# Optimization experiments

Hardware: AMD Instinct MI355X
Metric: run time of the kernel (lower is better)

## Reference

```python
import jax, jax.numpy as jnp
import numpy as np

CONTEXT_LENGTHS = [1, 3, 5, 7]
PADS = [(f - 1) // 2 for f in CONTEXT_LENGTHS]  # p(f) for odd f
B, H, L, DK = 2, 8, 1024, 64
C = H * DK  # conv channels = d_k * n_heads


def _conv1d(x, w, b, pad):
    # x: (b, C, L), w: (C, C, f), b: (C,) -- torch Conv1d semantics
    y = jax.lax.conv_general_dilated(
        x, w, window_strides=(1,), padding=[(pad, pad)],
        dimension_numbers=("NCH", "OIH", "NCH"))
    return y + b[None, :, None]


def _plane(a, w, b, pad, out_len):
    # Faithful to: conv(a.reshape(b, h*d_k, -1)).reshape(b, h, -1, d_k)[:, :, :out_len, :]
    bsz, h, l, d = a.shape
    y = _conv1d(a.reshape(bsz, h * d, l), w, b, pad)
    return y.reshape(bsz, h, -1, d)[:, :, :out_len, :]


def setup_inputs() -> dict:
    key = jax.random.key(0)
    ks = jax.random.split(key, 12)
    inp = {
        "Q": jax.random.normal(ks[0], (B, H, L, DK), jnp.float32),
        "K": jax.random.normal(ks[1], (B, H, L, DK), jnp.float32),
        "V": jax.random.normal(ks[2], (B, H, L, DK), jnp.float32),
        # causal mask: True = masked
        "attn_mask": jnp.broadcast_to(
            jnp.triu(jnp.ones((L, L), jnp.bool_), k=1), (B, H, L, L)),
    }
    for i, f in enumerate(CONTEXT_LENGTHS):
        scale = 1.0 / np.sqrt(C * f)
        inp[f"conv_w{i}"] = jax.random.normal(ks[3 + i], (C, C, f), jnp.float32) * scale
        inp[f"conv_b{i}"] = jax.random.normal(ks[7 + i], (C,), jnp.float32) * scale
    return inp


def reference(Q, K, V, attn_mask,
              conv_w0, conv_b0, conv_w1, conv_b1,
              conv_w2, conv_b2, conv_w3, conv_b3):
    ws = [conv_w0, conv_w1, conv_w2, conv_w3]
    bs = [conv_b0, conv_b1, conv_b2, conv_b3]
    b, h, l, d_k = Q.shape
    l_k = K.shape[2]
    p = len(CONTEXT_LENGTHS)
    Q_l = [_plane(Q, ws[i], bs[i], PADS[i], l) for i in range(p)]
    K_l = [_plane(K, ws[i], bs[i], PADS[i], l_k) for i in range(p)]
    # replicate torch.cat(dim=0).reshape(b, h, p, l, d) exactly (row-major)
    Q_p = jnp.concatenate(Q_l, axis=0).reshape(b, h, p, l, d_k)
    K_p = jnp.concatenate(K_l, axis=0).reshape(b, h, p, l_k, d_k)
    scores = jnp.einsum("bhpqd,bhpkd->bhpqk", Q_p, K_p) / np.sqrt(d_k).astype(np.float32)
    scores = jnp.where(attn_mask[:, :, None, :, :], jnp.float32(-1e9), scores)
    attn = jax.nn.softmax(scores, axis=-1)
    attn = jnp.max(attn, axis=2)  # max over planes -> (b,h,q,k)
    context = jnp.einsum("bhqk,bhkd->bhqd", attn, V)
    return (context, attn)
```

## Files before the change

kernel.cpp:

```cpp
#include <hip/hip_runtime.h>
#include <math.h>

#define C_CH 512
#define L_SEQ 1024
#define DK 64
#define NP 4
#define SC2 0.1803368801111f

typedef __attribute__((ext_vector_type(8))) short short8;
typedef __attribute__((ext_vector_type(4))) float f32x4;

__device__ __forceinline__ unsigned short f2bf(float f) {
    union { float f; unsigned u; } v; v.f = f;
    unsigned u = v.u;
    u += 0x7FFFu + ((u >> 16) & 1u);
    return (unsigned short)(u >> 16);
}

__global__ __launch_bounds__(256)
void prep_w_kernel(const float* __restrict__ w0, const float* __restrict__ w1,
                   const float* __restrict__ w2, const float* __restrict__ w3,
                   unsigned short* __restrict__ Wb) {
    int tg = blockIdx.y;
    int plane, t;
    if (tg < 1)      { plane = 0; t = tg; }
    else if (tg < 4) { plane = 1; t = tg - 1; }
    else if (tg < 9) { plane = 2; t = tg - 4; }
    else             { plane = 3; t = tg - 9; }
    const float* W = (plane == 0) ? w0 : (plane == 1) ? w1 : (plane == 2) ? w2 : w3;
    const int f = (plane == 0) ? 1 : (plane == 1) ? 3 : (plane == 2) ? 5 : 7;

    int co = blockIdx.x * 32 + (threadIdx.x >> 3);
    int c8 = threadIdx.x & 7;
    for (int it = 0; it < 8; it++) {
        int ci = c8 * 8 + it * 64;
        unsigned short o[8];
#pragma unroll
        for (int j = 0; j < 8; j++)
            o[j] = f2bf(W[(size_t)(co * C_CH + ci + j) * f + t]);
        *(short8*)&Wb[((size_t)tg * C_CH + co) * C_CH + ci] = *(short8*)o;
    }
}

__global__ __launch_bounds__(256)
void prep_x_kernel(const float* __restrict__ Qin, const float* __restrict__ Kin,
                   unsigned short* __restrict__ Xt) {
    int tb = blockIdx.z;
    int tensor = tb >> 1, b = tb & 1;
    const float* X = (tensor ? Kin : Qin) + (size_t)b * C_CH * L_SEQ;
    unsigned short* O = Xt + (size_t)tb * 1032 * C_CH;

    int pos0 = blockIdx.x * 64;
    int ci0  = blockIdx.y * 64;
    int tid = threadIdx.x;

    __shared__ float tile[64][65];
    int tx = tid & 15, ty = tid >> 4;
#pragma unroll
    for (int rr = 0; rr < 4; rr++) {
        int ci_l = ty + rr * 16;
        float4 v = *(const float4*)&X[(size_t)(ci0 + ci_l) * L_SEQ + pos0 + tx * 4];
        tile[tx * 4 + 0][ci_l] = v.x;
        tile[tx * 4 + 1][ci_l] = v.y;
        tile[tx * 4 + 2][ci_l] = v.z;
        tile[tx * 4 + 3][ci_l] = v.w;
    }
    __syncthreads();
#pragma unroll
    for (int pp = 0; pp < 2; pp++) {
        int pos_l = (tid >> 3) + pp * 32;
        int cg = (tid & 7) * 8;
        unsigned short o[8];
#pragma unroll
        for (int j = 0; j < 8; j++) o[j] = f2bf(tile[pos_l][cg + j]);
        *(short8*)&O[(size_t)(pos0 + pos_l + 4) * C_CH + ci0 + cg] = *(short8*)o;
    }
    if (blockIdx.x == 0) {
        int r = tid >> 6, cc = tid & 63;
        O[(size_t)r * C_CH + ci0 + cc] = 0;
    }
    if (blockIdx.x == 15) {
        int r = tid >> 6, cc = tid & 63;
        O[(size_t)(1028 + r) * C_CH + ci0 + cc] = 0;
    }
}

__global__ __launch_bounds__(256)
void conv_pair_kernel(const unsigned short* __restrict__ Xt,
                      const unsigned short* __restrict__ Wb,
                      const float* __restrict__ b0, const float* __restrict__ b1,
                      const float* __restrict__ b2, const float* __restrict__ b3,
                      unsigned short* __restrict__ Qp, unsigned short* __restrict__ Kp) {
    const int fs[4]   = {1, 3, 5, 7};
    const int toff[4] = {0, 1, 4, 9};
    int blk = blockIdx.x;
    int cls = blk >> 7;
    int idx = blk & 127;
    int co0  = (idx & 3) * 128;
    int pos0 = ((idx >> 2) & 7) * 128;
    int tb   = idx >> 5;
    int tensor = tb >> 1, b = tb & 1;
    unsigned short* Out = tensor ? Kp : Qp;
    const unsigned short* Xbase = Xt + (size_t)tb * 1032 * C_CH;

    __shared__ __align__(16) unsigned short As[4096];
    __shared__ __align__(16) unsigned short Bs[4096];

    int tid  = threadIdx.x;
    int w    = tid >> 6;
    int lane = tid & 63;
    int l15  = lane & 15;
    int quad = lane >> 4;
    int wm = (w & 1) * 64;
    int wn = (w >> 1) * 64;
    int rowL = tid >> 2;
    int cS   = tid & 3;

    int woff[2];
#pragma unroll
    for (int rep = 0; rep < 2; rep++) {
        int r = rowL + rep * 64;
        int line = r >> 1;
        int sl = (((r & 1) << 2) | cS) ^ (line & 7);
        woff[rep] = line * 64 + sl * 8;
    }
    int aoff[4], boff[4];
#pragma unroll
    for (int mi = 0; mi < 4; mi++) {
        int r = wm + mi * 16 + l15;
        int line = r >> 1;
        aoff[mi] = line * 64 + ((((r & 1) << 2) | quad) ^ (line & 7)) * 8;
        int r2 = wn + mi * 16 + l15;
        int line2 = r2 >> 1;
        boff[mi] = line2 * 64 + ((((r2 & 1) << 2) | quad) ^ (line2 & 7)) * 8;
    }

    for (int ti = 0; ti < 2; ti++) {
        int plane = (cls == 0) ? (ti == 0 ? 0 : 3) : (ti == 0 ? 1 : 2);
        const int f   = fs[plane];
        const int pad = (f - 1) >> 1;
        const float* bias = (plane == 0) ? b0 : (plane == 1) ? b1 : (plane == 2) ? b2 : b3;
        const int n = f * 16;

        f32x4 acc[4][4];
#pragma unroll
        for (int mi = 0; mi < 4; mi++)
#pragma unroll
            for (int ni = 0; ni < 4; ni++) acc[mi][ni] = (f32x4){0.f, 0.f, 0.f, 0.f};

        short8 pA[2], pB[2];
        {
            const unsigned short* Wsl = Wb + ((size_t)toff[plane] * C_CH + co0) * C_CH;
            const unsigned short* Xsl = Xbase + (size_t)(pos0 - pad + 4) * C_CH;
#pragma unroll
            for (int rep = 0; rep < 2; rep++) {
                int r = rowL + rep * 64;
                pA[rep] = *(const short8*)&Wsl[(size_t)r * C_CH + cS * 8];
                pB[rep] = *(const short8*)&Xsl[(size_t)r * C_CH + cS * 8];
            }
        }

        for (int it = 0; it < n; it++) {
            __syncthreads();
            *(short8*)&As[woff[0]] = pA[0];
            *(short8*)&As[woff[1]] = pA[1];
            *(short8*)&Bs[woff[0]] = pB[0];
            *(short8*)&Bs[woff[1]] = pB[1];
            __syncthreads();

            if (it + 1 < n) {
                int t = (it + 1) >> 4, cc = (it + 1) & 15;
                const unsigned short* Wsl =
                    Wb + ((size_t)(toff[plane] + t) * C_CH + co0) * C_CH + cc * 32;
                const unsigned short* Xsl =
                    Xbase + (size_t)(pos0 + t - pad + 4) * C_CH + cc * 32;
#pragma unroll
                for (int rep = 0; rep < 2; rep++) {
                    int r = rowL + rep * 64;
                    pA[rep] = *(const short8*)&Wsl[(size_t)r * C_CH + cS * 8];
                    pB[rep] = *(const short8*)&Xsl[(size_t)r * C_CH + cS * 8];
                }
            }

            short8 af[4], bf[4];
#pragma unroll
            for (int mi = 0; mi < 4; mi++) af[mi] = *(const short8*)&As[aoff[mi]];
#pragma unroll
            for (int ni = 0; ni < 4; ni++) bf[ni] = *(const short8*)&Bs[boff[ni]];
#pragma unroll
            for (int mi = 0; mi < 4; mi++)
#pragma unroll
                for (int ni = 0; ni < 4; ni++)
                    acc[mi][ni] = __builtin_amdgcn_mfma_f32_16x16x32_bf16(
                        af[mi], bf[ni], acc[mi][ni], 0, 0, 0);
        }

#pragma unroll
        for (int mi = 0; mi < 4; mi++)
#pragma unroll
            for (int r = 0; r < 4; r++) {
                int co = co0 + wm + mi * 16 + quad * 4 + r;
                int h = co >> 6, cl = co & 63;
                float bv = bias[co];
                size_t sbase = (size_t)((b * 8 + h) * NP + plane) * L_SEQ * DK;
#pragma unroll
                for (int ni = 0; ni < 4; ni++) {
                    int pos = pos0 + wn + ni * 16 + l15;
                    int l = cl * 16 + (pos >> 6);
                    int d = pos & 63;
                    Out[sbase + (size_t)l * DK + d] = f2bf(acc[mi][ni][r] + bv);
                }
            }
    }
}

__global__ __launch_bounds__(256)
void attn_stats_kernel(const unsigned short* __restrict__ Qb,
                       const unsigned short* __restrict__ Kb,
                       float* __restrict__ pstats) {
    int kc = blockIdx.x, qt = blockIdx.y, bh = blockIdx.z;
    int tid = threadIdx.x;
    size_t pbase = ((size_t)(bh * 16 + qt) * 4 + kc) * (NP * 64);

    if (kc * 4 > qt) { pstats[pbase + tid] = 0.f; return; }

    int q0 = qt * 64;
    int b2 = bh >> 3, h2 = bh & 7;
    int plane  = b2 * 2 + (h2 >> 2);
    int b_orig = (h2 >> 1) & 1;
    int h_base = (h2 & 1) * 4;
    int w = tid >> 6, lane = tid & 63, l15 = lane & 15, quad = lane >> 4;

    const unsigned short* kbase[NP];
    short8 qa[NP][2];
#pragma unroll
    for (int p = 0; p < NP; p++) {
        size_t slice = (size_t)((b_orig * 8 + h_base + p) * NP + plane);
        kbase[p] = Kb + slice * L_SEQ * DK;
        const unsigned short* qrow =
            Qb + (slice * L_SEQ + (size_t)(q0 + w * 16 + l15)) * DK + quad * 8;
        qa[p][0] = *(const short8*)(qrow);
        qa[p][1] = *(const short8*)(qrow + 32);
    }

    float l[NP][4];
#pragma unroll
    for (int p = 0; p < NP; p++)
        for (int r = 0; r < 4; r++) l[p][r] = 0.f;

    int kt1 = min(kc * 4 + 3, qt);
    for (int kt = kc * 4; kt <= kt1; kt++) {
        int k0 = kt * 64;
        bool diag = (kt == qt);
#pragma unroll
        for (int p = 0; p < NP; p++) {
            f32x4 c[4];
#pragma unroll
            for (int s = 0; s < 4; s++) {
                const unsigned short* kr =
                    kbase[p] + (size_t)(k0 + s * 16 + l15) * DK + quad * 8;
                short8 kb0 = *(const short8*)(kr);
                short8 kb1 = *(const short8*)(kr + 32);
                f32x4 acc = {0.f, 0.f, 0.f, 0.f};
                acc = __builtin_amdgcn_mfma_f32_16x16x32_bf16(qa[p][0], kb0, acc, 0, 0, 0);
                acc = __builtin_amdgcn_mfma_f32_16x16x32_bf16(qa[p][1], kb1, acc, 0, 0, 0);
                c[s] = acc;
            }
#pragma unroll
            for (int r = 0; r < 4; r++) {
                int row_local = quad * 4 + r + w * 16;
#pragma unroll
                for (int s = 0; s < 4; s++) {
                    float x = c[s][r] * SC2;
                    if (diag && (s * 16 + l15 > row_local)) x = -1e30f;
                    l[p][r] += exp2f(x);
                }
            }
        }
    }

#pragma unroll
    for (int p = 0; p < NP; p++)
#pragma unroll
        for (int r = 0; r < 4; r++) {
            float ll = l[p][r];
            ll += __shfl_xor(ll, 1);
            ll += __shfl_xor(ll, 2);
            ll += __shfl_xor(ll, 4);
            ll += __shfl_xor(ll, 8);
            if (l15 == 0)
                pstats[pbase + p * 64 + (w * 16 + quad * 4 + r)] = ll;
        }
}

__global__ __launch_bounds__(256)
void attn_combine_kernel(const float* __restrict__ pstats,
                         float* __restrict__ fstats,
                         float* __restrict__ out_ctx) {
    int qt = blockIdx.x, bh = blockIdx.y;
    int tid = threadIdx.x;
    size_t base = ((size_t)(bh * 16 + qt) * 4) * (NP * 64);

    float l = 0.f;
#pragma unroll
    for (int kc = 0; kc < 4; kc++)
        l += pstats[base + (size_t)kc * (NP * 64) + tid];
    fstats[(size_t)(bh * 16 + qt) * (NP * 64) + tid] = __log2f(l);

    int r = tid >> 2, c = (tid & 3) * 16;
    float4 z = make_float4(0.f, 0.f, 0.f, 0.f);
    size_t cbase = ((size_t)bh * L_SEQ + qt * 64 + r) * DK + c;
#pragma unroll
    for (int j = 0; j < 4; j++)
        *(float4*)&out_ctx[cbase + j * 4] = z;
}

__global__ __launch_bounds__(256)
void attn_apply_kernel(const unsigned short* __restrict__ Qb,
                       const unsigned short* __restrict__ Kb,
                       const float* __restrict__ V,
                       const float* __restrict__ fstats,
                       float* __restrict__ out_ctx, float* __restrict__ out_attn) {
    int kc = blockIdx.x, qt = blockIdx.y, bh = blockIdx.z;
    int tid = threadIdx.x;
    int q0 = qt * 64;
    bool any = (kc * 4 <= qt);

    int b2 = bh >> 3, h2 = bh & 7;
    int plane  = b2 * 2 + (h2 >> 2);
    int b_orig = (h2 >> 1) & 1;
    int h_base = (h2 & 1) * 4;
    int w = tid >> 6, lane = tid & 63, l15 = lane & 15, quad = lane >> 4;

    __shared__ float zsm[NP * 64];
    __shared__ __align__(16) unsigned short ast[64 * 80];
    __shared__ __align__(16) unsigned short vts[64 * 80];

    const unsigned short* kbase[NP];
    short8 qa[NP][2];
    if (any) {
        zsm[tid] = fstats[(size_t)(bh * 16 + qt) * (NP * 64) + tid];
#pragma unroll
        for (int p = 0; p < NP; p++) {
            size_t slice = (size_t)((b_orig * 8 + h_base + p) * NP + plane);
            kbase[p] = Kb + slice * L_SEQ * DK;
            const unsigned short* qrow =
                Qb + (slice * L_SEQ + (size_t)(q0 + w * 16 + l15)) * DK + quad * 8;
            qa[p][0] = *(const short8*)(qrow);
            qa[p][1] = *(const short8*)(qrow + 32);
        }
    }

    f32x4 ctxc[4];
#pragma unroll
    for (int ds = 0; ds < 4; ds++) ctxc[ds] = (f32x4){0.f, 0.f, 0.f, 0.f};

    for (int k4 = 0; k4 < 4; k4++) {
        int kt = kc * 4 + k4;
        int k0 = kt * 64;

        if (kt > qt) {
            float4 z = make_float4(0.f, 0.f, 0.f, 0.f);
            size_t abase = ((size_t)bh * L_SEQ + q0) * L_SEQ + k0;
#pragma unroll
            for (int j = 0; j < 4; j++) {
                int flat = tid + j * 256;
                *(float4*)&out_attn[abase + (size_t)(flat >> 4) * L_SEQ + (flat & 15) * 4] = z;
            }
            continue;
        }
        bool diag = (kt == qt);

        __syncthreads();

        {
            int kl = tid >> 2, db = (tid & 3) * 16;
            const float* vr = V + ((size_t)bh * L_SEQ + k0 + kl) * DK + db;
            float vv[16];
            *(float4*)&vv[0]  = *(const float4*)(vr);
            *(float4*)&vv[4]  = *(const float4*)(vr + 4);
            *(float4*)&vv[8]  = *(const float4*)(vr + 8);
            *(float4*)&vv[12] = *(const float4*)(vr + 12);
#pragma unroll
            for (int j = 0; j < 16; j++)
                vts[(db + j) * 80 + kl] = f2bf(vv[j]);
        }

        float run[4][4];
#pragma unroll
        for (int s = 0; s < 4; s++)
            for (int r = 0; r < 4; r++) run[s][r] = -1e30f;

#pragma unroll
        for (int p = 0; p < NP; p++) {
            f32x4 c[4];
#pragma unroll
            for (int s = 0; s < 4; s++) {
                const unsigned short* kr =
                    kbase[p] + (size_t)(k0 + s * 16 + l15) * DK + quad * 8;
                short8 kb0 = *(const short8*)(kr);
                short8 kb1 = *(const short8*)(kr + 32);
                f32x4 acc = {0.f, 0.f, 0.f, 0.f};
                acc = __builtin_amdgcn_mfma_f32_16x16x32_bf16(qa[p][0], kb0, acc, 0, 0, 0);
                acc = __builtin_amdgcn_mfma_f32_16x16x32_bf16(qa[p][1], kb1, acc, 0, 0, 0);
                c[s] = acc;
            }
#pragma unroll
            for (int r = 0; r < 4; r++) {
                float zp = zsm[p * 64 + (quad * 4 + r + w * 16)];
#pragma unroll
                for (int s = 0; s < 4; s++)
                    run[s][r] = fmaxf(run[s][r], c[s][r] * SC2 - zp);
            }
        }

#pragma unroll
        for (int s = 0; s < 4; s++)
#pragma unroll
            for (int r = 0; r < 4; r++) {
                int qloc = w * 16 + quad * 4 + r;
                bool masked = diag && (s * 16 + l15 > qloc);
                float a = masked ? 0.f : exp2f(run[s][r]);
                out_attn[((size_t)bh * L_SEQ + q0 + qloc) * L_SEQ + k0 + s * 16 + l15] = a;
                ast[qloc * 80 + s * 16 + l15] = f2bf(a);
            }
        __syncthreads();

        short8 af0 = *(const short8*)&ast[(w * 16 + l15) * 80 + quad * 8];
        short8 af1 = *(const short8*)&ast[(w * 16 + l15) * 80 + 32 + quad * 8];
#pragma unroll
        for (int ds = 0; ds < 4; ds++) {
            short8 bf0 = *(const short8*)&vts[(ds * 16 + l15) * 80 + quad * 8];
            short8 bf1 = *(const short8*)&vts[(ds * 16 + l15) * 80 + 32 + quad * 8];
            ctxc[ds] = __builtin_amdgcn_mfma_f32_16x16x32_bf16(af0, bf0, ctxc[ds], 0, 0, 0);
            ctxc[ds] = __builtin_amdgcn_mfma_f32_16x16x32_bf16(af1, bf1, ctxc[ds], 0, 0, 0);
        }
    }

    if (any) {
#pragma unroll
        for (int ds = 0; ds < 4; ds++)
#pragma unroll
            for (int r = 0; r < 4; r++) {
                int qg = q0 + w * 16 + quad * 4 + r;
                unsafeAtomicAdd(&out_ctx[((size_t)bh * L_SEQ + qg) * DK + ds * 16 + l15],
                                ctxc[ds][r]);
            }
    }
}

extern "C" void kernel_launch(void* const* d_in, const int* in_sizes, int n_in,
                              void* d_out, int out_size, void* d_ws, size_t ws_size,
                              hipStream_t stream) {
    const float* Q  = (const float*)d_in[0];
    const float* K  = (const float*)d_in[1];
    const float* V  = (const float*)d_in[2];
    const float* w0 = (const float*)d_in[4];
    const float* b0 = (const float*)d_in[5];
    const float* w1 = (const float*)d_in[6];
    const float* b1 = (const float*)d_in[7];
    const float* w2 = (const float*)d_in[8];
    const float* b2 = (const float*)d_in[9];
    const float* w3 = (const float*)d_in[10];
    const float* b3 = (const float*)d_in[11];

    char* ws = (char*)d_ws;
    unsigned short* Wb = (unsigned short*)(ws);
    unsigned short* Xt = (unsigned short*)(ws + 8388608);
    unsigned short* Qp = (unsigned short*)(ws + 12615680);
    unsigned short* Kp = (unsigned short*)(ws + 21004288);
    float* pstats = (float*)(ws + 8388608);
    float* fstats = (float*)(ws + 8388608 + 1048576);

    float* out_ctx  = (float*)d_out;
    float* out_attn = out_ctx + 1048576;

    prep_w_kernel<<<dim3(16, 16), 256, 0, stream>>>(w0, w1, w2, w3, Wb);
    prep_x_kernel<<<dim3(16, 8, 4), 256, 0, stream>>>(Q, K, Xt);
    conv_pair_kernel<<<dim3(256), 256, 0, stream>>>(Xt, Wb, b0, b1, b2, b3, Qp, Kp);
    attn_stats_kernel<<<dim3(4, 16, 16), 256, 0, stream>>>(Qp, Kp, pstats);
    attn_combine_kernel<<<dim3(16, 16), 256, 0, stream>>>(pstats, fstats, out_ctx);
    attn_apply_kernel<<<dim3(4, 16, 16), 256, 0, stream>>>(Qp, Kp, V, fstats,
                                                           out_ctx, out_attn);
}
```

Before: 365.6 us.

## Split conv per plane with double-buffered LDS, triangular tile grids for attention

The conv kernel now launches one block per plane tile (512 blocks) instead of pairing planes per block, and double-buffers the LDS A/B tiles so only one barrier per K-step is needed. Both attention kernels switch to a triangular grid over (q-tile, k-tile) pairs, which skips fully masked tiles instead of launching and early-exiting them. Row sums are now accumulated with atomics into a memset buffer, and the upper-triangle zeroing of the attention output moves into the combine kernel. This adds more atomics and an extra memset in exchange for better load balance and more parallelism.

```diff
diff --git a/kernel.cpp b/kernel.cpp
--- a/kernel.cpp
+++ b/kernel.cpp
@@ -15,6 +15,14 @@
     unsigned u = v.u;
     u += 0x7FFFu + ((u >> 16) & 1u);
     return (unsigned short)(u >> 16);
+}
+
+__device__ __forceinline__ void unpack_tri(int t, int& qt, int& kt) {
+    int q = (int)((sqrtf(8.f * t + 1.f) - 1.f) * 0.5f);
+    while ((q + 1) * (q + 2) / 2 <= t) q++;
+    while (q * (q + 1) / 2 > t) q--;
+    qt = q;
+    kt = t - q * (q + 1) / 2;
 }
 
 __global__ __launch_bounds__(256)
@@ -86,25 +94,32 @@
 }
 
 __global__ __launch_bounds__(256)
-void conv_pair_kernel(const unsigned short* __restrict__ Xt,
+void conv_mfma_kernel(const unsigned short* __restrict__ Xt,
                       const unsigned short* __restrict__ Wb,
                       const float* __restrict__ b0, const float* __restrict__ b1,
                       const float* __restrict__ b2, const float* __restrict__ b3,
                       unsigned short* __restrict__ Qp, unsigned short* __restrict__ Kp) {
     const int fs[4]   = {1, 3, 5, 7};
     const int toff[4] = {0, 1, 4, 9};
-    int blk = blockIdx.x;
-    int cls = blk >> 7;
-    int idx = blk & 127;
-    int co0  = (idx & 3) * 128;
-    int pos0 = ((idx >> 2) & 7) * 128;
-    int tb   = idx >> 5;
+    int id = blockIdx.x;
+    int plane, rel;
+    if (id < 128)      { plane = 0; rel = id; }
+    else if (id < 256) { plane = 1; rel = id - 128; }
+    else if (id < 384) { plane = 3; rel = id - 256; }
+    else               { plane = 2; rel = id - 384; }
+    int co0  = (rel & 3) * 128;
+    int pos0 = ((rel >> 2) & 7) * 128;
+    int tb   = rel >> 5;
     int tensor = tb >> 1, b = tb & 1;
+    const int f   = fs[plane];
+    const int pad = (f - 1) >> 1;
+    const int n   = f * 16;
+    const float* bias = (plane == 0) ? b0 : (plane == 1) ? b1 : (plane == 2) ? b2 : b3;
     unsigned short* Out = tensor ? Kp : Qp;
     const unsigned short* Xbase = Xt + (size_t)tb * 1032 * C_CH;
 
-    __shared__ __align__(16) unsigned short As[4096];
-    __shared__ __align__(16) unsigned short Bs[4096];
+    __shared__ __align__(16) unsigned short As[2][4096];
+    __shared__ __align__(16) unsigned short Bs[2][4096];
 
     int tid  = threadIdx.x;
     int w    = tid >> 6;
@@ -135,23 +150,38 @@
         boff[mi] = line2 * 64 + ((((r2 & 1) << 2) | quad) ^ (line2 & 7)) * 8;
     }
 
-    for (int ti = 0; ti < 2; ti++) {
-        int plane = (cls == 0) ? (ti == 0 ? 0 : 3) : (ti == 0 ? 1 : 2);
-        const int f   = fs[plane];
-        const int pad = (f - 1) >> 1;
-        const float* bias = (plane == 0) ? b0 : (plane == 1) ? b1 : (plane == 2) ? b2 : b3;
-        const int n = f * 16;
-
-        f32x4 acc[4][4];
-#pragma unroll
-        for (int mi = 0; mi < 4; mi++)
-#pragma unroll
-            for (int ni = 0; ni < 4; ni++) acc[mi][ni] = (f32x4){0.f, 0.f, 0.f, 0.f};
-
-        short8 pA[2], pB[2];
-        {
-            const unsigned short* Wsl = Wb + ((size_t)toff[plane] * C_CH + co0) * C_CH;
-            const unsigned short* Xsl = Xbase + (size_t)(pos0 - pad + 4) * C_CH;
+    f32x4 acc[4][4];
+#pragma unroll
+    for (int mi = 0; mi < 4; mi++)
+#pragma unroll
+        for (int ni = 0; ni < 4; ni++) acc[mi][ni] = (f32x4){0.f, 0.f, 0.f, 0.f};
+
+    short8 pA[2], pB[2];
+    {
+        const unsigned short* Wsl = Wb + ((size_t)toff[plane] * C_CH + co0) * C_CH;
+        const unsigned short* Xsl = Xbase + (size_t)(pos0 - pad + 4) * C_CH;
+#pragma unroll
+        for (int rep = 0; rep < 2; rep++) {
+            int r = rowL + rep * 64;
+            pA[rep] = *(const short8*)&Wsl[(size_t)r * C_CH + cS * 8];
+            pB[rep] = *(const short8*)&Xsl[(size_t)r * C_CH + cS * 8];
+        }
+    }
+
+    for (int it = 0; it < n; it++) {
+        int cur = it & 1;
+        *(short8*)&As[cur][woff[0]] = pA[0];
+        *(short8*)&As[cur][woff[1]] = pA[1];
+        *(short8*)&Bs[cur][woff[0]] = pB[0];
+        *(short8*)&Bs[cur][woff[1]] = pB[1];
+        __syncthreads();
+
+        if (it + 1 < n) {
+            int t = (it + 1) >> 4, cc = (it + 1) & 15;
+            const unsigned short* Wsl =
+                Wb + ((size_t)(toff[plane] + t) * C_CH + co0) * C_CH + cc * 32;
+            const unsigned short* Xsl =
+                Xbase + (size_t)(pos0 + t - pad + 4) * C_CH + cc * 32;
 #pragma unroll
             for (int rep = 0; rep < 2; rep++) {
                 int r = rowL + rep * 64;
@@ -160,76 +190,152 @@
             }
         }
 
-        for (int it = 0; it < n; it++) {
-            __syncthreads();
-            *(short8*)&As[woff[0]] = pA[0];
-            *(short8*)&As[woff[1]] = pA[1];
-            *(short8*)&Bs[woff[0]] = pB[0];
-            *(short8*)&Bs[woff[1]] = pB[1];
-            __syncthreads();
-
-            if (it + 1 < n) {
-                int t = (it + 1) >> 4, cc = (it + 1) & 15;
-                const unsigned short* Wsl =
-                    Wb + ((size_t)(toff[plane] + t) * C_CH + co0) * C_CH + cc * 32;
-                const unsigned short* Xsl =
-                    Xbase + (size_t)(pos0 + t - pad + 4) * C_CH + cc * 32;
-#pragma unroll
-                for (int rep = 0; rep < 2; rep++) {
-                    int r = rowL + rep * 64;
-                    pA[rep] = *(const short8*)&Wsl[(size_t)r * C_CH + cS * 8];
-                    pB[rep] = *(const short8*)&Xsl[(size_t)r * C_CH + cS * 8];
-                }
+        short8 af[4], bf[4];
+#pragma unroll
+        for (int mi = 0; mi < 4; mi++) af[mi] = *(const short8*)&As[cur][aoff[mi]];
+#pragma unroll
+        for (int ni = 0; ni < 4; ni++) bf[ni] = *(const short8*)&Bs[cur][boff[ni]];
+#pragma unroll
+        for (int mi = 0; mi < 4; mi++)
+#pragma unroll
+            for (int ni = 0; ni < 4; ni++)
+                acc[mi][ni] = __builtin_amdgcn_mfma_f32_16x16x32_bf16(
+                    af[mi], bf[ni], acc[mi][ni], 0, 0, 0);
+    }
+
+#pragma unroll
+    for (int mi = 0; mi < 4; mi++)
+#pragma unroll
+        for (int r = 0; r < 4; r++) {
+            int co = co0 + wm + mi * 16 + quad * 4 + r;
+            int h = co >> 6, cl = co & 63;
+            float bv = bias[co];
+            size_t sbase = (size_t)((b * 8 + h) * NP + plane) * L_SEQ * DK;
+#pragma unroll
+            for (int ni = 0; ni < 4; ni++) {
+                int pos = pos0 + wn + ni * 16 + l15;
+                int l = cl * 16 + (pos >> 6);
+                int d = pos & 63;
+                Out[sbase + (size_t)l * DK + d] = f2bf(acc[mi][ni][r] + bv);
             }
-
-            short8 af[4], bf[4];
-#pragma unroll
-            for (int mi = 0; mi < 4; mi++) af[mi] = *(const short8*)&As[aoff[mi]];
-#pragma unroll
-            for (int ni = 0; ni < 4; ni++) bf[ni] = *(const short8*)&Bs[boff[ni]];
-#pragma unroll
-            for (int mi = 0; mi < 4; mi++)
-#pragma unroll
-                for (int ni = 0; ni < 4; ni++)
-                    acc[mi][ni] = __builtin_amdgcn_mfma_f32_16x16x32_bf16(
-                        af[mi], bf[ni], acc[mi][ni], 0, 0, 0);
-        }
-
-#pragma unroll
-        for (int mi = 0; mi < 4; mi++)
-#pragma unroll
-            for (int r = 0; r < 4; r++) {
-                int co = co0 + wm + mi * 16 + quad * 4 + r;
-                int h = co >> 6, cl = co & 63;
-                float bv = bias[co];
-                size_t sbase = (size_t)((b * 8 + h) * NP + plane) * L_SEQ * DK;
-#pragma unroll
-                for (int ni = 0; ni < 4; ni++) {
-                    int pos = pos0 + wn + ni * 16 + l15;
-                    int l = cl * 16 + (pos >> 6);
-                    int d = pos & 63;
-                    Out[sbase + (size_t)l * DK + d] = f2bf(acc[mi][ni][r] + bv);
-                }
-            }
-    }
+        }
 }
 
 __global__ __launch_bounds__(256)
 void attn_stats_kernel(const unsigned short* __restrict__ Qb,
                        const unsigned short* __restrict__ Kb,
-                       float* __restrict__ pstats) {
-    int kc = blockIdx.x, qt = blockIdx.y, bh = blockIdx.z;
+                       float* __restrict__ lsum) {
+    int qt, kt;
+    unpack_tri(blockIdx.x, qt, kt);
+    int bh = blockIdx.y;
     int tid = threadIdx.x;
-    size_t pbase = ((size_t)(bh * 16 + qt) * 4 + kc) * (NP * 64);
-
-    if (kc * 4 > qt) { pstats[pbase + tid] = 0.f; return; }
-
-    int q0 = qt * 64;
+    int q0 = qt * 64, k0 = kt * 64;
+    bool diag = (kt == qt);
+
     int b2 = bh >> 3, h2 = bh & 7;
     int plane  = b2 * 2 + (h2 >> 2);
     int b_orig = (h2 >> 1) & 1;
     int h_base = (h2 & 1) * 4;
     int w = tid >> 6, lane = tid & 63, l15 = lane & 15, quad = lane >> 4;
+
+    float l[NP][4];
+#pragma unroll
+    for (int p = 0; p < NP; p++)
+        for (int r = 0; r < 4; r++) l[p][r] = 0.f;
+
+#pragma unroll
+    for (int p = 0; p < NP; p++) {
+        size_t slice = (size_t)((b_orig * 8 + h_base + p) * NP + plane);
+        const unsigned short* kb = Kb + slice * L_SEQ * DK;
+        const unsigned short* qrow =
+            Qb + (slice * L_SEQ + (size_t)(q0 + w * 16 + l15)) * DK + quad * 8;
+        short8 qa0 = *(const short8*)(qrow);
+        short8 qa1 = *(const short8*)(qrow + 32);
+
+        f32x4 c[4];
+#pragma unroll
+        for (int s = 0; s < 4; s++) {
+            const unsigned short* kr = kb + (size_t)(k0 + s * 16 + l15) * DK + quad * 8;
+            short8 kb0 = *(const short8*)(kr);
+            short8 kb1 = *(const short8*)(kr + 32);
+            f32x4 acc = {0.f, 0.f, 0.f, 0.f};
+            acc = __builtin_amdgcn_mfma_f32_16x16x32_bf16(qa0, kb0, acc, 0, 0, 0);
+            acc = __builtin_amdgcn_mfma_f32_16x16x32_bf16(qa1, kb1, acc, 0, 0, 0);
+            c[s] = acc;
+        }
+#pragma unroll
+        for (int r = 0; r < 4; r++) {
+            int row_local = quad * 4 + r + w * 16;
+#pragma unroll
+            for (int s = 0; s < 4; s++) {
+                float x = c[s][r] * SC2;
+                if (diag && (s * 16 + l15 > row_local)) x = -1e30f;
+                l[p][r] += exp2f(x);
+            }
+        }
+    }
+
+    size_t base = (size_t)(bh * 16 + qt) * (NP * 64);
+#pragma unroll
+    for (int p = 0; p < NP; p++)
+#pragma unroll
+        for (int r = 0; r < 4; r++) {
+            float ll = l[p][r];
+            ll += __shfl_xor(ll, 1);
+            ll += __shfl_xor(ll, 2);
+            ll += __shfl_xor(ll, 4);
+            ll += __shfl_xor(ll, 8);
+            if (l15 == 0)
+                unsafeAtomicAdd(&lsum[base + p * 64 + (w * 16 + quad * 4 + r)], ll);
+        }
+}
+
+__global__ __launch_bounds__(256)
+void attn_combine_kernel(const float* __restrict__ lsum,
+                         float* __restrict__ fstats,
+                         float* __restrict__ out_ctx, float* __restrict__ out_attn) {
+    int qt = blockIdx.x, bh = blockIdx.y;
+    int tid = threadIdx.x;
+    size_t sb = (size_t)(bh * 16 + qt) * (NP * 64);
+    fstats[sb + tid] = __log2f(lsum[sb + tid]);
+
+    int r = tid >> 2, c = (tid & 3) * 16;
+    float4 z = make_float4(0.f, 0.f, 0.f, 0.f);
+    size_t cbase = ((size_t)bh * L_SEQ + qt * 64 + r) * DK + c;
+#pragma unroll
+    for (int j = 0; j < 4; j++)
+        *(float4*)&out_ctx[cbase + j * 4] = z;
+
+    int kz = (qt + 1) * 64;
+    size_t abase = ((size_t)bh * L_SEQ + qt * 64 + r) * L_SEQ;
+    for (int k = kz + (tid & 3) * 4; k < L_SEQ; k += 16)
+        *(float4*)&out_attn[abase + k] = z;
+}
+
+__global__ __launch_bounds__(256)
+void attn_apply_kernel(const unsigned short* __restrict__ Qb,
+                       const unsigned short* __restrict__ Kb,
+                       const float* __restrict__ V,
+                       const float* __restrict__ fstats,
+                       float* __restrict__ out_ctx, float* __restrict__ out_attn) {
+    int qt, kt;
+    unpack_tri(blockIdx.x, qt, kt);
+    int bh = blockIdx.y;
+    int tid = threadIdx.x;
+    int q0 = qt * 64, k0 = kt * 64;
+    bool diag = (kt == qt);
+
+    int b2 = bh >> 3, h2 = bh & 7;
+    int plane  = b2 * 2 + (h2 >> 2);
+    int b_orig = (h2 >> 1) & 1;
+    int h_base = (h2 & 1) * 4;
+    int w = tid >> 6, lane = tid & 63, l15 = lane & 15, quad = lane >> 4;
+
+    __shared__ float zsm[NP * 64];
+    __shared__ __align__(16) unsigned short ast[64 * 80];
+    __shared__ __align__(16) unsigned short vts[64 * 80];
+
+    zsm[tid] = fstats[(size_t)(bh * 16 + qt) * (NP * 64) + tid];
 
     const unsigned short* kbase[NP];
     short8 qa[NP][2];
@@ -243,210 +349,80 @@
         qa[p][1] = *(const short8*)(qrow + 32);
     }
 
-    float l[NP][4];
-#pragma unroll
-    for (int p = 0; p < NP; p++)
-        for (int r = 0; r < 4; r++) l[p][r] = 0.f;
-
-    int kt1 = min(kc * 4 + 3, qt);
-    for (int kt = kc * 4; kt <= kt1; kt++) {
-        int k0 = kt * 64;
-        bool diag = (kt == qt);
-#pragma unroll
-        for (int p = 0; p < NP; p++) {
-            f32x4 c[4];
-#pragma unroll
-            for (int s = 0; s < 4; s++) {
-                const unsigned short* kr =
-                    kbase[p] + (size_t)(k0 + s * 16 + l15) * DK + quad * 8;
-                short8 kb0 = *(const short8*)(kr);
-                short8 kb1 = *(const short8*)(kr + 32);
-                f32x4 acc = {0.f, 0.f, 0.f, 0.f};
-                acc = __builtin_amdgcn_mfma_f32_16x16x32_bf16(qa[p][0], kb0, acc, 0, 0, 0);
-                acc = __builtin_amdgcn_mfma_f32_16x16x32_bf16(qa[p][1], kb1, acc, 0, 0, 0);
-                c[s] = acc;
-            }
-#pragma unroll
-            for (int r = 0; r < 4; r++) {
-                int row_local = quad * 4 + r + w * 16;
-#pragma unroll
-                for (int s = 0; s < 4; s++) {
-                    float x = c[s][r] * SC2;
-                    if (diag && (s * 16 + l15 > row_local)) x = -1e30f;
-                    l[p][r] += exp2f(x);
-                }
-            }
-        }
-    }
-
-#pragma unroll
-    for (int p = 0; p < NP; p++)
-#pragma unroll
-        for (int r = 0; r < 4; r++) {
-            float ll = l[p][r];
-            ll += __shfl_xor(ll, 1);
-            ll += __shfl_xor(ll, 2);
-            ll += __shfl_xor(ll, 4);
-            ll += __shfl_xor(ll, 8);
-            if (l15 == 0)
-                pstats[pbase + p * 64 + (w * 16 + quad * 4 + r)] = ll;
-        }
-}
-
-__global__ __launch_bounds__(256)
-void attn_combine_kernel(const float* __restrict__ pstats,
-                         float* __restrict__ fstats,
-                         float* __restrict__ out_ctx) {
-    int qt = blockIdx.x, bh = blockIdx.y;
-    int tid = threadIdx.x;
-    size_t base = ((size_t)(bh * 16 + qt) * 4) * (NP * 64);
-
-    float l = 0.f;
-#pragma unroll
-    for (int kc = 0; kc < 4; kc++)
-        l += pstats[base + (size_t)kc * (NP * 64) + tid];
-    fstats[(size_t)(bh * 16 + qt) * (NP * 64) + tid] = __log2f(l);
-
-    int r = tid >> 2, c = (tid & 3) * 16;
-    float4 z = make_float4(0.f, 0.f, 0.f, 0.f);
-    size_t cbase = ((size_t)bh * L_SEQ + qt * 64 + r) * DK + c;
-#pragma unroll
-    for (int j = 0; j < 4; j++)
-        *(float4*)&out_ctx[cbase + j * 4] = z;
-}
-
-__global__ __launch_bounds__(256)
-void attn_apply_kernel(const unsigned short* __restrict__ Qb,
-                       const unsigned short* __restrict__ Kb,
-                       const float* __restrict__ V,
-                       const float* __restrict__ fstats,
-                       float* __restrict__ out_ctx, float* __restrict__ out_attn) {
-    int kc = blockIdx.x, qt = blockIdx.y, bh = blockIdx.z;
-    int tid = threadIdx.x;
-    int q0 = qt * 64;
-    bool any = (kc * 4 <= qt);
-
-    int b2 = bh >> 3, h2 = bh & 7;
-    int plane  = b2 * 2 + (h2 >> 2);
-    int b_orig = (h2 >> 1) & 1;
-    int h_base = (h2 & 1) * 4;
-    int w = tid >> 6, lane = tid & 63, l15 = lane & 15, quad = lane >> 4;
-
-    __shared__ float zsm[NP * 64];
-    __shared__ __align__(16) unsigned short ast[64 * 80];
-    __shared__ __align__(16) unsigned short vts[64 * 80];
-
-    const unsigned short* kbase[NP];
-    short8 qa[NP][2];
-    if (any) {
-        zsm[tid] = fstats[(size_t)(bh * 16 + qt) * (NP * 64) + tid];
-#pragma unroll
-        for (int p = 0; p < NP; p++) {
-            size_t slice = (size_t)((b_orig * 8 + h_base + p) * NP + plane);
-            kbase[p] = Kb + slice * L_SEQ * DK;
-            const unsigned short* qrow =
-                Qb + (slice * L_SEQ + (size_t)(q0 + w * 16 + l15)) * DK + quad * 8;
-            qa[p][0] = *(const short8*)(qrow);
-            qa[p][1] = *(const short8*)(qrow + 32);
-        }
-    }
+    {
+        int kl = tid >> 2, db = (tid & 3) * 16;
+        const float* vr = V + ((size_t)bh * L_SEQ + k0 + kl) * DK + db;
+        float vv[16];
+        *(float4*)&vv[0]  = *(const float4*)(vr);
+        *(float4*)&vv[4]  = *(const float4*)(vr + 4);
+        *(float4*)&vv[8]  = *(const float4*)(vr + 8);
+        *(float4*)&vv[12] = *(const float4*)(vr + 12);
+#pragma unroll
+        for (int j = 0; j < 16; j++)
+            vts[(db + j) * 80 + kl] = f2bf(vv[j]);
+    }
+    __syncthreads();
+
+    float run[4][4];
+#pragma unroll
+    for (int s = 0; s < 4; s++)
+        for (int r = 0; r < 4; r++) run[s][r] = -1e30f;
+
+#pragma unroll
+    for (int p = 0; p < NP; p++) {
+        f32x4 c[4];
+#pragma unroll
+        for (int s = 0; s < 4; s++) {
+            const unsigned short* kr =
+                kbase[p] + (size_t)(k0 + s * 16 + l15) * DK + quad * 8;
+            short8 kb0 = *(const short8*)(kr);
+            short8 kb1 = *(const short8*)(kr + 32);
+            f32x4 acc = {0.f, 0.f, 0.f, 0.f};
+            acc = __builtin_amdgcn_mfma_f32_16x16x32_bf16(qa[p][0], kb0, acc, 0, 0, 0);
+            acc = __builtin_amdgcn_mfma_f32_16x16x32_bf16(qa[p][1], kb1, acc, 0, 0, 0);
+            c[s] = acc;
+        }
+#pragma unroll
+        for (int r = 0; r < 4; r++) {
+            float zp = zsm[p * 64 + (quad * 4 + r + w * 16)];
+#pragma unroll
+            for (int s = 0; s < 4; s++)
+                run[s][r] = fmaxf(run[s][r], c[s][r] * SC2 - zp);
+        }
+    }
+
+#pragma unroll
+    for (int s = 0; s < 4; s++)
+#pragma unroll
+        for (int r = 0; r < 4; r++) {
+            int qloc = w * 16 + quad * 4 + r;
+            bool masked = diag && (s * 16 + l15 > qloc);
+            float a = masked ? 0.f : exp2f(run[s][r]);
+            out_attn[((size_t)bh * L_SEQ + q0 + qloc) * L_SEQ + k0 + s * 16 + l15] = a;
+            ast[qloc * 80 + s * 16 + l15] = f2bf(a);
+        }
 
     f32x4 ctxc[4];
 #pragma unroll
     for (int ds = 0; ds < 4; ds++) ctxc[ds] = (f32x4){0.f, 0.f, 0.f, 0.f};
-
-    for (int k4 = 0; k4 < 4; k4++) {
-        int kt = kc * 4 + k4;
-        int k0 = kt * 64;
-
-        if (kt > qt) {
-            float4 z = make_float4(0.f, 0.f, 0.f, 0.f);
-            size_t abase = ((size_t)bh * L_SEQ + q0) * L_SEQ + k0;
-#pragma unroll
-            for (int j = 0; j < 4; j++) {
-                int flat = tid + j * 256;
-                *(float4*)&out_attn[abase + (size_t)(flat >> 4) * L_SEQ + (flat & 15) * 4] = z;
-            }
-            continue;
-        }
-        bool diag = (kt == qt);
-
-        __syncthreads();
-
-        {
-            int kl = tid >> 2, db = (tid & 3) * 16;
-            const float* vr = V + ((size_t)bh * L_SEQ + k0 + kl) * DK + db;
-            float vv[16];
-            *(float4*)&vv[0]  = *(const float4*)(vr);
-            *(float4*)&vv[4]  = *(const float4*)(vr + 4);
-            *(float4*)&vv[8]  = *(const float4*)(vr + 8);
-            *(float4*)&vv[12] = *(const float4*)(vr + 12);
-#pragma unroll
-            for (int j = 0; j < 16; j++)
-                vts[(db + j) * 80 + kl] = f2bf(vv[j]);
-        }
-
-        float run[4][4];
-#pragma unroll
-        for (int s = 0; s < 4; s++)
-            for (int r = 0; r < 4; r++) run[s][r] = -1e30f;
-
-#pragma unroll
-        for (int p = 0; p < NP; p++) {
-            f32x4 c[4];
-#pragma unroll
-            for (int s = 0; s < 4; s++) {
-                const unsigned short* kr =
-                    kbase[p] + (size_t)(k0 + s * 16 + l15) * DK + quad * 8;
-                short8 kb0 = *(const short8*)(kr);
-                short8 kb1 = *(const short8*)(kr + 32);
-                f32x4 acc = {0.f, 0.f, 0.f, 0.f};
-                acc = __builtin_amdgcn_mfma_f32_16x16x32_bf16(qa[p][0], kb0, acc, 0, 0, 0);
-                acc = __builtin_amdgcn_mfma_f32_16x16x32_bf16(qa[p][1], kb1, acc, 0, 0, 0);
-                c[s] = acc;
-            }
-#pragma unroll
-            for (int r = 0; r < 4; r++) {
-                float zp = zsm[p * 64 + (quad * 4 + r + w * 16)];
-#pragma unroll
-                for (int s = 0; s < 4; s++)
-                    run[s][r] = fmaxf(run[s][r], c[s][r] * SC2 - zp);
-            }
-        }
-
-#pragma unroll
-        for (int s = 0; s < 4; s++)
-#pragma unroll
-            for (int r = 0; r < 4; r++) {
-                int qloc = w * 16 + quad * 4 + r;
-                bool masked = diag && (s * 16 + l15 > qloc);
-                float a = masked ? 0.f : exp2f(run[s][r]);
-                out_attn[((size_t)bh * L_SEQ + q0 + qloc) * L_SEQ + k0 + s * 16 + l15] = a;
-                ast[qloc * 80 + s * 16 + l15] = f2bf(a);
-            }
-        __syncthreads();
-
-        short8 af0 = *(const short8*)&ast[(w * 16 + l15) * 80 + quad * 8];
-        short8 af1 = *(const short8*)&ast[(w * 16 + l15) * 80 + 32 + quad * 8];
-#pragma unroll
-        for (int ds = 0; ds < 4; ds++) {
-            short8 bf0 = *(const short8*)&vts[(ds * 16 + l15) * 80 + quad * 8];
-            short8 bf1 = *(const short8*)&vts[(ds * 16 + l15) * 80 + 32 + quad * 8];
-            ctxc[ds] = __builtin_amdgcn_mfma_f32_16x16x32_bf16(af0, bf0, ctxc[ds], 0, 0, 0);
-            ctxc[ds] = __builtin_amdgcn_mfma_f32_16x16x32_bf16(af1, bf1, ctxc[ds], 0, 0, 0);
-        }
-    }
-
-    if (any) {
-#pragma unroll
-        for (int ds = 0; ds < 4; ds++)
-#pragma unroll
-            for (int r = 0; r < 4; r++) {
-                int qg = q0 + w * 16 + quad * 4 + r;
-                unsafeAtomicAdd(&out_ctx[((size_t)bh * L_SEQ + qg) * DK + ds * 16 + l15],
-                                ctxc[ds][r]);
-            }
-    }
+    short8 af0 = *(const short8*)&ast[(w * 16 + l15) * 80 + quad * 8];
+    short8 af1 = *(const short8*)&ast[(w * 16 + l15) * 80 + 32 + quad * 8];
+#pragma unroll
+    for (int ds = 0; ds < 4; ds++) {
+        short8 bf0 = *(const short8*)&vts[(ds * 16 + l15) * 80 + quad * 8];
+        short8 bf1 = *(const short8*)&vts[(ds * 16 + l15) * 80 + 32 + quad * 8];
+        ctxc[ds] = __builtin_amdgcn_mfma_f32_16x16x32_bf16(af0, bf0, ctxc[ds], 0, 0, 0);
+        ctxc[ds] = __builtin_amdgcn_mfma_f32_16x16x32_bf16(af1, bf1, ctxc[ds], 0, 0, 0);
+    }
+
+#pragma unroll
+    for (int ds = 0; ds < 4; ds++)
+#pragma unroll
+        for (int r = 0; r < 4; r++) {
+            int qg = q0 + w * 16 + quad * 4 + r;
+            unsafeAtomicAdd(&out_ctx[((size_t)bh * L_SEQ + qg) * DK + ds * 16 + l15],
+                            ctxc[ds][r]);
+        }
 }
 
 extern "C" void kernel_launch(void* const* d_in, const int* in_sizes, int n_in,
@@ -469,17 +445,18 @@
     unsigned short* Xt = (unsigned short*)(ws + 8388608);
     unsigned short* Qp = (unsigned short*)(ws + 12615680);
     unsigned short* Kp = (unsigned short*)(ws + 21004288);
-    float* pstats = (float*)(ws + 8388608);
-    float* fstats = (float*)(ws + 8388608 + 1048576);
+    float* lsum   = (float*)(ws + 8388608);
+    float* fstats = (float*)(ws + 8388608 + 262144);
 
     float* out_ctx  = (float*)d_out;
     float* out_attn = out_ctx + 1048576;
 
     prep_w_kernel<<<dim3(16, 16), 256, 0, stream>>>(w0, w1, w2, w3, Wb);
     prep_x_kernel<<<dim3(16, 8, 4), 256, 0, stream>>>(Q, K, Xt);
-    conv_pair_kernel<<<dim3(256), 256, 0, stream>>>(Xt, Wb, b0, b1, b2, b3, Qp, Kp);
-    attn_stats_kernel<<<dim3(4, 16, 16), 256, 0, stream>>>(Qp, Kp, pstats);
-    attn_combine_kernel<<<dim3(16, 16), 256, 0, stream>>>(pstats, fstats, out_ctx);
-    attn_apply_kernel<<<dim3(4, 16, 16), 256, 0, stream>>>(Qp, Kp, V, fstats,
-                                                           out_ctx, out_attn);
-}
+    conv_mfma_kernel<<<dim3(512), 256, 0, stream>>>(Xt, Wb, b0, b1, b2, b3, Qp, Kp);
+    hipMemsetAsync(lsum, 0, 262144, stream);
+    attn_stats_kernel<<<dim3(136, 16), 256, 0, stream>>>(Qp, Kp, lsum);
+    attn_combine_kernel<<<dim3(16, 16), 256, 0, stream>>>(lsum, fstats, out_ctx, out_attn);
+    attn_apply_kernel<<<dim3(136, 16), 256, 0, stream>>>(Qp, Kp, V, fstats,
+                                                         out_ctx, out_attn);
+}
```

Result: faster. 355.0 us (-2.9%).
